# Performance work log

Measured on AMD Instinct MI355X. Metric: run time of the kernel, lower is better.

Reference implementation:

```python
import jax, jax.numpy as jnp
import numpy as np
from math import sqrt

B, TS_D, SEG, D, H = 16, 2, 1024, 256, 8
D_FF = 1024
DK = D // H
EPS = 1e-5


def _layernorm(x, g, b):
    mu = jnp.mean(x, axis=-1, keepdims=True)
    var = jnp.mean(jnp.square(x - mu), axis=-1, keepdims=True)
    return (x - mu) * jax.lax.rsqrt(var + EPS) * g + b


def setup_inputs() -> dict:
    key = jax.random.key(0)
    ks = jax.random.split(key, 16)
    s = 0.02
    return {
        "x": jax.random.normal(ks[0], (B, TS_D, SEG, D), dtype=jnp.float32),
        "Wq": jax.random.normal(ks[1], (D, D), dtype=jnp.float32) * s,
        "bq": jnp.zeros((D,), jnp.float32),
        "Wk": jax.random.normal(ks[2], (D, D), dtype=jnp.float32) * s,
        "bk": jnp.zeros((D,), jnp.float32),
        "Wv": jax.random.normal(ks[3], (D, D), dtype=jnp.float32) * s,
        "bv": jnp.zeros((D,), jnp.float32),
        "Wo": jax.random.normal(ks[4], (D, D), dtype=jnp.float32) * s,
        "bo": jnp.zeros((D,), jnp.float32),
        "g31": jnp.ones((D,), jnp.float32),
        "b31": jnp.zeros((D,), jnp.float32),
        "W1": jax.random.normal(ks[5], (D, D_FF), dtype=jnp.float32) * s,
        "b1": jnp.zeros((D_FF,), jnp.float32),
        "W2": jax.random.normal(ks[6], (D_FF, D), dtype=jnp.float32) * s,
        "b2": jnp.zeros((D,), jnp.float32),
        "g41": jnp.ones((D,), jnp.float32),
        "b41": jnp.zeros((D,), jnp.float32),
    }


def reference(x, Wq, bq, Wk, bk, Wv, bv, Wo, bo, g31, b31, W1, b1, W2, b2, g41, b41):
    # x: [B, ts_d=2, seg, d]; output is final_out2 (only live path of the module)
    b, ts_d, seg, d = x.shape
    scale = 1.0 / sqrt(DK)
    segments = x.reshape(b, ts_d * seg, d)            # [B, 2*seg, d]
    Q = (segments @ Wq + bq).reshape(b, -1, H, DK)
    K = (segments @ Wk + bk).reshape(b, -1, H, DK)
    V = (segments @ Wv + bv).reshape(b, -1, H, DK)
    q = Q[:, :seg]       # first seg positions (channel 0)
    k = K[:, -seg:]      # last seg positions (channel 1)
    v = V[:, -seg:]
    # cross-segment dual attention
    A1 = jax.nn.softmax(scale * jnp.einsum('blhe,bshe->bhls', q, k), axis=-1)
    out1 = jnp.einsum('bhls,bshd->blhd', A1, v).reshape(b, seg, d)
    A2 = jax.nn.softmax(scale * jnp.einsum('blhe,bshe->bhls', k, q), axis=-1)
    out2 = jnp.einsum('bhls,bshd->blhd', A2, q).reshape(b, seg, d)
    y = jnp.concatenate([out1, out2], axis=1) @ Wo + bo   # [B, 2*seg, d]
    h = _layernorm(segments + y, g31, b31)
    mlp = jax.nn.gelu(h @ W1 + b1, approximate=False) @ W2 + b2
    h = _layernorm(h + mlp, g41, b41)
    return h.reshape(b, ts_d, seg, d)
```

## Files before the change

kernel.cpp:

```cpp
#include <hip/hip_runtime.h>
#include <hip/hip_bf16.h>
#include <math.h>

#define BATCH 16
#define SEG 1024
#define DMODEL 256
#define NH 8
#define DK 32
#define DFF 1024
#define NTOK (BATCH * 2 * SEG)
#define EPS 1e-5f

typedef __attribute__((ext_vector_type(8))) short short8;
typedef __attribute__((ext_vector_type(4))) short short4b;
typedef __attribute__((ext_vector_type(4))) float f32x4;

#if __has_builtin(__builtin_amdgcn_exp2f)
#define EXP2(x) __builtin_amdgcn_exp2f(x)
#else
#define EXP2(x) __expf((x) * 0.6931471805599453f)
#endif

__device__ __forceinline__ ushort f2bf(float x) {
    union { float f; unsigned u; } a; a.f = x;
    unsigned r = a.u + 0x7fffu + ((a.u >> 16) & 1u);
    return (ushort)(r >> 16);
}

typedef const __attribute__((address_space(1))) unsigned gas_u32;
typedef __attribute__((address_space(3))) unsigned las_u32;
__device__ __forceinline__ void gload_lds16(const ushort* g, ushort* l) {
    __builtin_amdgcn_global_load_lds((gas_u32*)g, (las_u32*)l, 16, 0, 0);
}

__global__ __launch_bounds__(256) void wfrag_kernel(
    const float* __restrict__ src, ushort* __restrict__ dst, int K, int N, int order)
{
    const int tid = blockIdx.x * 256 + threadIdx.x;
    const int KT_ = K >> 5, NT_ = N >> 4;
    const int total = KT_ * NT_ * 64;
    if (tid >= total) return;
    const int lane = tid & 63;
    const int frag = tid >> 6;
    int kt, nt;
    if (order) { kt = frag / NT_; nt = frag % NT_; }
    else       { nt = frag / KT_; kt = frag % KT_; }
    const int quad = lane >> 4, l = lane & 15;
    const float* s = src + (size_t)(kt * 32 + quad * 8) * N + nt * 16 + l;
    short8 v;
#pragma unroll
    for (int j = 0; j < 8; j++) v[j] = (short)f2bf(s[(size_t)j * N]);
    *(short8*)&dst[(size_t)tid * 8] = v;
}

#define ASTR 264

__device__ __forceinline__ void dense256_pass(
    const ushort* __restrict__ Wf, ushort* WL, const short8* af,
    f32x4* acc, int t, int w, int lane)
{
#pragma unroll
    for (int nt = 0; nt < 16; ++nt) acc[nt] = (f32x4){0.f, 0.f, 0.f, 0.f};
    for (int c = 0; c < 4; ++c) {
        const ushort* g = Wf + (size_t)c * 16384 + w * 4096 + lane * 8;
        ushort* ld = WL + w * 4096;
#pragma unroll
        for (int i = 0; i < 8; ++i) gload_lds16(g + i * 512, ld + i * 512);
        __syncthreads();
#pragma unroll
        for (int n2 = 0; n2 < 4; ++n2)
#pragma unroll
            for (int kt = 0; kt < 8; ++kt) {
                const short8 bf_ = *(const short8*)&WL[(n2 * 8 + kt) * 512 + lane * 8];
                acc[c * 4 + n2] = __builtin_amdgcn_mfma_f32_16x16x32_bf16(af[kt], bf_, acc[c * 4 + n2], 0, 0, 0);
            }
        __syncthreads();
    }
}

__global__ __launch_bounds__(256) void qkv_mfma_kernel(
    const float* __restrict__ x,
    const ushort* __restrict__ Wqf, const float* __restrict__ bq,
    const ushort* __restrict__ Wkf, const float* __restrict__ bk,
    const ushort* __restrict__ Wvf, const float* __restrict__ bv,
    ushort* __restrict__ qbuf, ushort* __restrict__ kbuf,
    ushort* __restrict__ qt, ushort* __restrict__ vt)
{
    __shared__ __align__(16) ushort SM[64 * ASTR];
    const int bid = blockIdx.x;
    const int half = bid >> 8;
    const int sub = bid & 255;
    const int b = sub >> 4, ti = sub & 15;
    const int t = threadIdx.x;
    const int w = t >> 6, lane = t & 63, l = lane & 15, quad = lane >> 4;

    const float* xrow = x + ((size_t)b * 2048 + (size_t)half * 1024 + ti * 64) * 256;
#pragma unroll
    for (int p = 0; p < 16; ++p) {
        int ch = t + 256 * p;
        int row = ch >> 6, c4 = ch & 63;
        float4 v = *(const float4*)&xrow[row * 256 + c4 * 4];
        uint2 pk;
        pk.x = (unsigned)f2bf(v.x) | ((unsigned)f2bf(v.y) << 16);
        pk.y = (unsigned)f2bf(v.z) | ((unsigned)f2bf(v.w) << 16);
        *(uint2*)&SM[row * ASTR + c4 * 4] = pk;
    }
    __syncthreads();

    short8 af[8];
#pragma unroll
    for (int kt = 0; kt < 8; ++kt)
        af[kt] = *(const short8*)&SM[(w * 16 + l) * ASTR + kt * 32 + quad * 8];
    __syncthreads();

    f32x4 acc[16];
    const int npass = half ? 2 : 1;
    for (int pass = 0; pass < npass; ++pass) {
        const ushort* Wf = half ? (pass ? Wvf : Wkf) : Wqf;
        const float* bias = half ? (pass ? bv : bk) : bq;
        const float kscale = (half && pass == 0) ? 0.25503472f : 1.0f;
        dense256_pass(Wf, SM, af, acc, t, w, lane);

        ushort bfv[16][4];
#pragma unroll
        for (int nt = 0; nt < 16; ++nt) {
            const float bb = bias[nt * 16 + l];
#pragma unroll
            for (int r = 0; r < 4; ++r) bfv[nt][r] = f2bf((acc[nt][r] + bb) * kscale);
        }

        const bool rowout = (half == 0) || (pass == 0);
        const bool trout  = (half == 0) || (pass == 1);
        if (rowout) {
            ushort* obuf = half ? kbuf : qbuf;
#pragma unroll
            for (int nt = 0; nt < 16; ++nt) {
                const int h = nt >> 1, e = (nt & 1) * 16 + l;
#pragma unroll
                for (int r = 0; r < 4; ++r) {
                    int tok = ti * 64 + w * 16 + quad * 4 + r;
                    obuf[(((size_t)b * 8 + h) * SEG + tok) * 32 + e] = bfv[nt][r];
                }
            }
        }
        if (trout) {
            ushort* tb = half ? vt : qt;
#pragma unroll
            for (int nt = 0; nt < 16; ++nt)
#pragma unroll
                for (int r = 0; r < 4; ++r)
                    SM[(nt * 16 + l) * 66 + w * 16 + quad * 4 + r] = bfv[nt][r];
            __syncthreads();
            const int d = t, hh = t >> 5, e = t & 31;
            ushort* dr = tb + (((size_t)b * 8 + hh) * 32 + e) * 1024 + ti * 64;
#pragma unroll
            for (int j = 0; j < 8; ++j) {
                uint2 v;
                v.x = *(const unsigned*)&SM[d * 66 + j * 8];
                v.y = *(const unsigned*)&SM[d * 66 + j * 8 + 2];
                unsigned z0 = *(const unsigned*)&SM[d * 66 + j * 8 + 4];
                unsigned z1 = *(const unsigned*)&SM[d * 66 + j * 8 + 6];
                *(uint4*)&dr[j * 8] = make_uint4(v.x, v.y, z0, z1);
            }
            if (npass > pass + 1) __syncthreads();
        }
    }
}

#define KTILE 128
#define KP 40
#define VP 132

__global__ __launch_bounds__(256) void attn_mfma_kernel(
    const ushort* __restrict__ qbuf, const ushort* __restrict__ kbuf,
    const ushort* __restrict__ qt, const ushort* __restrict__ vt,
    ushort* __restrict__ abuf)
{
    __shared__ __align__(16) ushort Kl[KTILE * KP];
    __shared__ __align__(16) ushort Vl[32 * VP];

    const int bid   = blockIdx.x;
    const int sbh   = bid & 255;
    const int qtile = bid >> 8;
    const int stage = sbh >> 7;
    const int b     = (sbh >> 3) & 15;
    const int h     = sbh & 7;

    const ushort* Qm = stage ? kbuf : qbuf;
    const ushort* Km = stage ? qbuf : kbuf;
    const ushort* Vt = stage ? qt : vt;
    const size_t bh = ((size_t)b * 8 + h) * SEG * 32;

    const int t    = threadIdx.x;
    const int w    = t >> 6;
    const int lane = t & 63;
    const int l    = lane & 15;
    const int quad = lane >> 4;

    const int qrow = qtile * 64 + w * 16 + l;
    const short8 qf = *(const short8*)&Qm[bh + (size_t)qrow * 32 + quad * 8];

    f32x4 o0 = {0.f, 0.f, 0.f, 0.f};
    f32x4 o1 = {0.f, 0.f, 0.f, 0.f};
    f32x4 o2 = {0.f, 0.f, 0.f, 0.f};
    const short4b ones = {(short)0x3F80, (short)0x3F80, (short)0x3F80, (short)0x3F80};

    for (int tile = 0; tile < 8; ++tile) {
        __syncthreads();
        const ushort* Kg = &Km[bh + (size_t)(tile * KTILE) * 32];
#pragma unroll
        for (int p = 0; p < 2; ++p) {
            int ch = t + 256 * p;
            int row = ch >> 2, part = ch & 3;
            *(short8*)&Kl[row * KP + part * 8] = *(const short8*)&Kg[row * 32 + part * 8];
        }
        const ushort* Vg = &Vt[bh + (size_t)tile * KTILE];
#pragma unroll
        for (int p = 0; p < 2; ++p) {
            int ch = t + 256 * p;
            int d = ch >> 4, c = ch & 15;
            *(short8*)&Vl[d * VP + c * 8] = *(const short8*)&Vg[(size_t)d * 1024 + c * 8];
        }
        __syncthreads();

#pragma unroll
        for (int kb = 0; kb < 8; ++kb) {
            const short8 kf = *(const short8*)&Kl[(kb * 16 + l) * KP + quad * 8];
            f32x4 z = {0.f, 0.f, 0.f, 0.f};
            f32x4 sc = __builtin_amdgcn_mfma_f32_16x16x32_bf16(kf, qf, z, 0, 0, 0);
            union { float f; unsigned u; } a0, a1, a2, a3;
            a0.f = EXP2(sc[0]); a1.f = EXP2(sc[1]);
            a2.f = EXP2(sc[2]); a3.f = EXP2(sc[3]);
            unsigned lo = __builtin_amdgcn_perm(a1.u, a0.u, 0x07060302u);
            unsigned hi = __builtin_amdgcn_perm(a3.u, a2.u, 0x07060302u);
            union { uint2 u; short4b s; } pk; pk.u = make_uint2(lo, hi);
            const short4b vf0 = *(const short4b*)&Vl[l * VP + kb * 16 + quad * 4];
            const short4b vf1 = *(const short4b*)&Vl[(16 + l) * VP + kb * 16 + quad * 4];
            o0 = __builtin_amdgcn_mfma_f32_16x16x16bf16_1k(vf0, pk.s, o0, 0, 0, 0);
            o1 = __builtin_amdgcn_mfma_f32_16x16x16bf16_1k(vf1, pk.s, o1, 0, 0, 0);
            o2 = __builtin_amdgcn_mfma_f32_16x16x16bf16_1k(ones, pk.s, o2, 0, 0, 0);
        }
    }

    const float inv = 1.0f / o2[0];
#pragma unroll
    for (int r = 0; r < 4; ++r) { o0[r] *= inv; o1[r] *= inv; }

    __syncthreads();
    ushort* Ob = &Kl[w * 16 * 40];
#pragma unroll
    for (int r = 0; r < 4; ++r) {
        Ob[l * 40 + quad * 4 + r]      = f2bf(o0[r]);
        Ob[l * 40 + 16 + quad * 4 + r] = f2bf(o1[r]);
    }
    __syncthreads();
    const int q = lane >> 2, part = lane & 3;
    const short8 ov = *(const short8*)&Ob[q * 40 + part * 8];
    const int tok = qtile * 64 + w * 16 + q;
    *(short8*)&abuf[((size_t)b * 2 * SEG + (size_t)stage * SEG + tok) * 256 + h * 32 + part * 8] = ov;
}

__global__ __launch_bounds__(256) void proj_mfma_kernel(
    const ushort* __restrict__ abuf, const ushort* __restrict__ Wof,
    const float* __restrict__ bo, const float* __restrict__ x,
    const float* __restrict__ g31, const float* __restrict__ b31,
    float* __restrict__ hout)
{
    __shared__ __align__(16) ushort SM[64 * ASTR];
    const int bid = blockIdx.x;
    const size_t tok0 = (size_t)bid * 64;
    const int t = threadIdx.x;
    const int w = t >> 6, lane = t & 63, l = lane & 15, quad = lane >> 4;

#pragma unroll
    for (int p = 0; p < 8; ++p) {
        int ch = t + 256 * p;
        int row = ch >> 5, c8 = ch & 31;
        *(short8*)&SM[row * ASTR + c8 * 8] = *(const short8*)&abuf[(tok0 + row) * 256 + c8 * 8];
    }
    __syncthreads();

    short8 af[8];
#pragma unroll
    for (int kt = 0; kt < 8; ++kt)
        af[kt] = *(const short8*)&SM[(w * 16 + l) * ASTR + kt * 32 + quad * 8];
    __syncthreads();

    f32x4 acc[16];
    dense256_pass(Wof, SM, af, acc, t, w, lane);

#pragma unroll
    for (int nt = 0; nt < 16; ++nt) {
        const int d = nt * 16 + l;
        const float bv = bo[d];
#pragma unroll
        for (int r = 0; r < 4; ++r) {
            size_t tok = tok0 + w * 16 + quad * 4 + r;
            acc[nt][r] += bv + x[tok * 256 + d];
        }
    }

    float mu_[4], is_[4];
#pragma unroll
    for (int r = 0; r < 4; ++r) {
        float s = 0.f;
#pragma unroll
        for (int nt = 0; nt < 16; ++nt) s += acc[nt][r];
        s += __shfl_xor(s, 1); s += __shfl_xor(s, 2);
        s += __shfl_xor(s, 4); s += __shfl_xor(s, 8);
        float mu = s * (1.0f / 256.0f);
        float vs = 0.f;
#pragma unroll
        for (int nt = 0; nt < 16; ++nt) { float dd = acc[nt][r] - mu; vs += dd * dd; }
        vs += __shfl_xor(vs, 1); vs += __shfl_xor(vs, 2);
        vs += __shfl_xor(vs, 4); vs += __shfl_xor(vs, 8);
        mu_[r] = mu;
        is_[r] = rsqrtf(vs * (1.0f / 256.0f) + EPS);
    }

#pragma unroll
    for (int nt = 0; nt < 16; ++nt) {
        const int d = nt * 16 + l;
        const float gg = g31[d], bb = b31[d];
#pragma unroll
        for (int r = 0; r < 4; ++r) {
            size_t tok = tok0 + w * 16 + quad * 4 + r;
            hout[tok * 256 + d] = (acc[nt][r] - mu_[r]) * is_[r] * gg + bb;
        }
    }
}

#define GP 40

__global__ __launch_bounds__(256) void mlp_mfma_kernel(
    const float* __restrict__ W1dummy_unused, const ushort* __restrict__ W1f,
    const float* __restrict__ b1, const ushort* __restrict__ W2f,
    const float* __restrict__ b2, const float* __restrict__ g41,
    const float* __restrict__ b41, float* __restrict__ io)
{
    __shared__ __align__(16) ushort SM[64 * ASTR];
    __shared__ __align__(16) ushort G[4][16 * GP];
    const int bid = blockIdx.x;
    const size_t tok0 = (size_t)bid * 64;
    const int t = threadIdx.x;
    const int w = t >> 6, lane = t & 63, l = lane & 15, quad = lane >> 4;

    const float* hrow = io + tok0 * 256;
#pragma unroll
    for (int p = 0; p < 16; ++p) {
        int ch = t + 256 * p;
        int row = ch >> 6, c4 = ch & 63;
        float4 v = *(const float4*)&hrow[row * 256 + c4 * 4];
        uint2 pk;
        pk.x = (unsigned)f2bf(v.x) | ((unsigned)f2bf(v.y) << 16);
        pk.y = (unsigned)f2bf(v.z) | ((unsigned)f2bf(v.w) << 16);
        *(uint2*)&SM[row * ASTR + c4 * 4] = pk;
    }
    __syncthreads();

    short8 af[8];
#pragma unroll
    for (int kt = 0; kt < 8; ++kt)
        af[kt] = *(const short8*)&SM[(w * 16 + l) * ASTR + kt * 32 + quad * 8];
    __syncthreads();

    f32x4 out[16];
#pragma unroll
    for (int nt = 0; nt < 16; ++nt) out[nt] = (f32x4){0.f, 0.f, 0.f, 0.f};

    ushort* WL = &SM[0];
    ushort* Gw = &G[w][0];

    for (int c = 0; c < 32; ++c) {
        {
            const ushort* g1 = W1f + (size_t)c * 8192 + w * 2048 + lane * 8;
            ushort* l1 = WL + w * 2048;
            const ushort* g2 = W2f + (size_t)c * 8192 + w * 2048 + lane * 8;
            ushort* l2 = WL + 8192 + w * 2048;
#pragma unroll
            for (int i = 0; i < 4; ++i) {
                gload_lds16(g1 + i * 512, l1 + i * 512);
                gload_lds16(g2 + i * 512, l2 + i * 512);
            }
        }
        __syncthreads();

        f32x4 s[2];
        s[0] = (f32x4){0.f, 0.f, 0.f, 0.f};
        s[1] = (f32x4){0.f, 0.f, 0.f, 0.f};
#pragma unroll
        for (int n2 = 0; n2 < 2; ++n2)
#pragma unroll
            for (int kt = 0; kt < 8; ++kt) {
                const short8 bf_ = *(const short8*)&WL[(n2 * 8 + kt) * 512 + lane * 8];
                s[n2] = __builtin_amdgcn_mfma_f32_16x16x32_bf16(af[kt], bf_, s[n2], 0, 0, 0);
            }

#pragma unroll
        for (int n2 = 0; n2 < 2; ++n2) {
            const int ff = (c * 2 + n2) * 16 + l;
            const float bv = b1[ff];
#pragma unroll
            for (int r = 0; r < 4; ++r) {
                float v = s[n2][r] + bv;
                float gl = 0.5f * v * (1.0f + erff(v * 0.70710678118654752f));
                Gw[(quad * 4 + r) * GP + n2 * 16 + l] = f2bf(gl);
            }
        }

        const short8 gf = *(const short8*)&Gw[l * GP + quad * 8];
#pragma unroll
        for (int nt = 0; nt < 16; ++nt) {
            const short8 bf_ = *(const short8*)&WL[8192 + nt * 512 + lane * 8];
            out[nt] = __builtin_amdgcn_mfma_f32_16x16x32_bf16(gf, bf_, out[nt], 0, 0, 0);
        }
        __syncthreads();
    }

#pragma unroll
    for (int nt = 0; nt < 16; ++nt) {
        const int d = nt * 16 + l;
        const float bv = b2[d];
#pragma unroll
        for (int r = 0; r < 4; ++r) {
            size_t tok = tok0 + w * 16 + quad * 4 + r;
            out[nt][r] += bv + io[tok * 256 + d];
        }
    }

    float mu_[4], is_[4];
#pragma unroll
    for (int r = 0; r < 4; ++r) {
        float s = 0.f;
#pragma unroll
        for (int nt = 0; nt < 16; ++nt) s += out[nt][r];
        s += __shfl_xor(s, 1); s += __shfl_xor(s, 2);
        s += __shfl_xor(s, 4); s += __shfl_xor(s, 8);
        float mu = s * (1.0f / 256.0f);
        float vs = 0.f;
#pragma unroll
        for (int nt = 0; nt < 16; ++nt) { float dd = out[nt][r] - mu; vs += dd * dd; }
        vs += __shfl_xor(vs, 1); vs += __shfl_xor(vs, 2);
        vs += __shfl_xor(vs, 4); vs += __shfl_xor(vs, 8);
        mu_[r] = mu;
        is_[r] = rsqrtf(vs * (1.0f / 256.0f) + EPS);
    }

#pragma unroll
    for (int nt = 0; nt < 16; ++nt) {
        const int d = nt * 16 + l;
        const float gg = g41[d], bb = b41[d];
#pragma unroll
        for (int r = 0; r < 4; ++r) {
            size_t tok = tok0 + w * 16 + quad * 4 + r;
            io[tok * 256 + d] = (out[nt][r] - mu_[r]) * is_[r] * gg + bb;
        }
    }
}

extern "C" void kernel_launch(void* const* d_in, const int* in_sizes, int n_in,
                              void* d_out, int out_size, void* d_ws, size_t ws_size,
                              hipStream_t stream)
{
    const float* x   = (const float*)d_in[0];
    const float* Wq  = (const float*)d_in[1];
    const float* bq  = (const float*)d_in[2];
    const float* Wk  = (const float*)d_in[3];
    const float* bk  = (const float*)d_in[4];
    const float* Wv  = (const float*)d_in[5];
    const float* bv  = (const float*)d_in[6];
    const float* Wo  = (const float*)d_in[7];
    const float* bo  = (const float*)d_in[8];
    const float* g31 = (const float*)d_in[9];
    const float* b31 = (const float*)d_in[10];
    const float* W1  = (const float*)d_in[11];
    const float* b1  = (const float*)d_in[12];
    const float* W2  = (const float*)d_in[13];
    const float* b2  = (const float*)d_in[14];
    const float* g41 = (const float*)d_in[15];
    const float* b41 = (const float*)d_in[16];

    float* out = (float*)d_out;

    const size_t HALF = (size_t)BATCH * SEG * DMODEL;
    ushort* qbuf = (ushort*)d_ws;
    ushort* kbuf = qbuf + HALF;
    ushort* qt   = kbuf + HALF;
    ushort* vt   = qt + HALF;
    ushort* abuf = vt + HALF;
    ushort* Wqf  = abuf + 2 * HALF;
    ushort* Wkf  = Wqf + 65536;
    ushort* Wvf  = Wkf + 65536;
    ushort* Wof  = Wvf + 65536;
    ushort* W1f  = Wof + 65536;
    ushort* W2f  = W1f + 262144;

    wfrag_kernel<<<32, 256, 0, stream>>>(Wq, Wqf, 256, 256, 0);
    wfrag_kernel<<<32, 256, 0, stream>>>(Wk, Wkf, 256, 256, 0);
    wfrag_kernel<<<32, 256, 0, stream>>>(Wv, Wvf, 256, 256, 0);
    wfrag_kernel<<<32, 256, 0, stream>>>(Wo, Wof, 256, 256, 0);
    wfrag_kernel<<<128, 256, 0, stream>>>(W1, W1f, 256, 1024, 0);
    wfrag_kernel<<<128, 256, 0, stream>>>(W2, W2f, 1024, 256, 1);

    qkv_mfma_kernel<<<512, 256, 0, stream>>>(x, Wqf, bq, Wkf, bk, Wvf, bv,
                                             qbuf, kbuf, qt, vt);
    attn_mfma_kernel<<<2 * BATCH * NH * (SEG / 64), 256, 0, stream>>>(qbuf, kbuf, qt, vt, abuf);
    proj_mfma_kernel<<<NTOK / 64, 256, 0, stream>>>(abuf, Wof, bo, x, g31, b31, out);
    mlp_mfma_kernel<<<NTOK / 64, 256, 0, stream>>>(nullptr, W1f, b1, W2f, b2, g41, b41, out);
}
```

Measured before the change: 308.0 us.

## Double-buffer weight tiles in LDS and stage MLP bias in shared memory

The QKV/projection dense pass and the MLP kernel now load the first weight chunk before their loops. Each iteration then issues the async global-to-LDS load for the next chunk into the other buffer while running MFMAs on the current one. This hides global load latency behind compute and removes one barrier per iteration. The MLP kernel also caches b1 in LDS instead of reading it from global memory each chunk. The cost is roughly double the LDS use in the MLP kernel, which may reduce the number of resident blocks per CU.

```diff
diff --git a/kernel.cpp b/kernel.cpp
--- a/kernel.cpp
+++ b/kernel.cpp
@@ -61,17 +61,26 @@
 {
 #pragma unroll
     for (int nt = 0; nt < 16; ++nt) acc[nt] = (f32x4){0.f, 0.f, 0.f, 0.f};
+    {
+        const ushort* g = Wf + (size_t)w * 4096 + lane * 8;
+        ushort* ld = WL + w * 4096;
+#pragma unroll
+        for (int i = 0; i < 8; ++i) gload_lds16(g + i * 512, ld + i * 512);
+    }
+    __syncthreads();
     for (int c = 0; c < 4; ++c) {
-        const ushort* g = Wf + (size_t)c * 16384 + w * 4096 + lane * 8;
-        ushort* ld = WL + w * 4096;
-#pragma unroll
-        for (int i = 0; i < 8; ++i) gload_lds16(g + i * 512, ld + i * 512);
-        __syncthreads();
+        if (c < 3) {
+            const ushort* g = Wf + (size_t)(c + 1) * 16384 + w * 4096 + lane * 8;
+            ushort* ld = WL + ((c + 1) & 1) * 8192 + w * 4096;
+#pragma unroll
+            for (int i = 0; i < 8; ++i) gload_lds16(g + i * 512, ld + i * 512);
+        }
+        const ushort* buf = WL + (c & 1) * 8192;
 #pragma unroll
         for (int n2 = 0; n2 < 4; ++n2)
 #pragma unroll
             for (int kt = 0; kt < 8; ++kt) {
-                const short8 bf_ = *(const short8*)&WL[(n2 * 8 + kt) * 512 + lane * 8];
+                const short8 bf_ = *(const short8*)&buf[(n2 * 8 + kt) * 512 + lane * 8];
                 acc[c * 4 + n2] = __builtin_amdgcn_mfma_f32_16x16x32_bf16(af[kt], bf_, acc[c * 4 + n2], 0, 0, 0);
             }
         __syncthreads();
@@ -338,8 +347,9 @@
     const float* __restrict__ b2, const float* __restrict__ g41,
     const float* __restrict__ b41, float* __restrict__ io)
 {
-    __shared__ __align__(16) ushort SM[64 * ASTR];
+    __shared__ __align__(16) ushort SM[2 * 16384];
     __shared__ __align__(16) ushort G[4][16 * GP];
+    __shared__ __align__(16) float B1L[DFF];
     const int bid = blockIdx.x;
     const size_t tok0 = (size_t)bid * 64;
     const int t = threadIdx.x;
@@ -356,6 +366,7 @@
         pk.y = (unsigned)f2bf(v.z) | ((unsigned)f2bf(v.w) << 16);
         *(uint2*)&SM[row * ASTR + c4 * 4] = pk;
     }
+    *(float4*)&B1L[t * 4] = *(const float4*)&b1[t * 4];
     __syncthreads();
 
     short8 af[8];
@@ -368,22 +379,35 @@
 #pragma unroll
     for (int nt = 0; nt < 16; ++nt) out[nt] = (f32x4){0.f, 0.f, 0.f, 0.f};
 
-    ushort* WL = &SM[0];
     ushort* Gw = &G[w][0];
 
+    {
+        const ushort* g1 = W1f + w * 2048 + lane * 8;
+        const ushort* g2 = W2f + w * 2048 + lane * 8;
+        ushort* l1 = SM + w * 2048;
+        ushort* l2 = SM + 8192 + w * 2048;
+#pragma unroll
+        for (int i = 0; i < 4; ++i) {
+            gload_lds16(g1 + i * 512, l1 + i * 512);
+            gload_lds16(g2 + i * 512, l2 + i * 512);
+        }
+    }
+    __syncthreads();
+
     for (int c = 0; c < 32; ++c) {
-        {
-            const ushort* g1 = W1f + (size_t)c * 8192 + w * 2048 + lane * 8;
-            ushort* l1 = WL + w * 2048;
-            const ushort* g2 = W2f + (size_t)c * 8192 + w * 2048 + lane * 8;
-            ushort* l2 = WL + 8192 + w * 2048;
+        if (c < 31) {
+            const int nb = (c + 1) & 1;
+            const ushort* g1 = W1f + (size_t)(c + 1) * 8192 + w * 2048 + lane * 8;
+            ushort* l1 = SM + nb * 16384 + w * 2048;
+            const ushort* g2 = W2f + (size_t)(c + 1) * 8192 + w * 2048 + lane * 8;
+            ushort* l2 = SM + nb * 16384 + 8192 + w * 2048;
 #pragma unroll
             for (int i = 0; i < 4; ++i) {
                 gload_lds16(g1 + i * 512, l1 + i * 512);
                 gload_lds16(g2 + i * 512, l2 + i * 512);
             }
         }
-        __syncthreads();
+        const ushort* WL = SM + (c & 1) * 16384;
 
         f32x4 s[2];
         s[0] = (f32x4){0.f, 0.f, 0.f, 0.f};
@@ -398,8 +422,7 @@
 
 #pragma unroll
         for (int n2 = 0; n2 < 2; ++n2) {
-            const int ff = (c * 2 + n2) * 16 + l;
-            const float bv = b1[ff];
+            const float bv = B1L[c * 32 + n2 * 16 + l];
 #pragma unroll
             for (int r = 0; r < 4; ++r) {
                 float v = s[n2][r] + bv;
```

Measured after the change: 289.8 us. 5.9% less time.
